# Performance work log

Hardware: AMD Instinct MI355X
Metric: run time of the kernel (lower is better)

The kernel has to match this reference:

```python
import jax, jax.numpy as jnp
import numpy as np

B, OBS, D_MODEL, D_STATE, D_CONV, EXPAND, ACT = 2048, 512, 1024, 16, 4, 2, 18
D_INNER = EXPAND * D_MODEL            # 2048
DT_RANK = (D_MODEL + 15) // 16        # 64

def setup_inputs() -> dict:
    key = jax.random.key(0)
    ks = jax.random.split(key, 20)
    s = 0.02
    return {
        "obs": jax.random.normal(ks[0], (B, OBS), jnp.float32),
        "conv_state": jax.random.normal(ks[1], (B, D_INNER, D_CONV), jnp.float32),
        "ssm_state": jax.random.normal(ks[2], (B, D_INNER, D_STATE), jnp.float32),
        # obs -> d_model projection
        "in_proj_w": jax.random.normal(ks[3], (D_MODEL, OBS), jnp.float32) * s,
        "in_proj_b": jnp.zeros((D_MODEL,), jnp.float32),
        # Mamba in_proj (no bias): d_model -> 2*d_inner (x and z)
        "mamba_in_w": jax.random.normal(ks[4], (2 * D_INNER, D_MODEL), jnp.float32) * s,
        # depthwise causal conv
        "conv_w": jax.random.normal(ks[5], (D_INNER, D_CONV), jnp.float32) * s,
        "conv_b": jnp.zeros((D_INNER,), jnp.float32),
        # x_proj (no bias): d_inner -> dt_rank + 2*d_state
        "x_proj_w": jax.random.normal(ks[6], (DT_RANK + 2 * D_STATE, D_INNER), jnp.float32) * s,
        # dt_proj: dt_rank -> d_inner
        "dt_w": jax.random.normal(ks[7], (D_INNER, DT_RANK), jnp.float32) * s,
        "dt_b": jax.random.normal(ks[8], (D_INNER,), jnp.float32) * s,
        # S4D-style A init: A_log = log(A), A in [1, d_state]
        "A_log": jnp.log(jnp.broadcast_to(jnp.arange(1, D_STATE + 1, dtype=jnp.float32), (D_INNER, D_STATE)) + 0.0),
        "D": jnp.ones((D_INNER,), jnp.float32),
        # out_proj (no bias): d_inner -> d_model
        "out_proj_w": jax.random.normal(ks[9], (D_MODEL, D_INNER), jnp.float32) * s,
        # actor / critic heads
        "pol_w": jax.random.normal(ks[10], (ACT, D_MODEL), jnp.float32) * s,
        "pol_b": jnp.zeros((ACT,), jnp.float32),
        "val_w": jax.random.normal(ks[11], (1, D_MODEL), jnp.float32) * s,
        "val_b": jnp.zeros((1,), jnp.float32),
    }

def _silu(x):
    return x * jax.nn.sigmoid(x)

def reference(obs, conv_state, ssm_state, in_proj_w, in_proj_b, mamba_in_w,
              conv_w, conv_b, x_proj_w, dt_w, dt_b, A_log, D, out_proj_w,
              pol_w, pol_b, val_w, val_b):
    # obs projection: [B, d_model]
    h = obs @ in_proj_w.T + in_proj_b
    # Mamba step (single timestep)
    xz = h @ mamba_in_w.T                        # [B, 2*d_inner]
    x, z = xz[:, :D_INNER], xz[:, D_INNER:]
    # causal depthwise conv via shifted conv_state buffer
    conv_state_new = jnp.concatenate([conv_state[:, :, 1:], x[:, :, None]], axis=-1)  # [B, d_inner, d_conv]
    x = _silu(jnp.sum(conv_state_new * conv_w[None], axis=-1) + conv_b)               # [B, d_inner]
    # input-dependent dt, B, C
    x_db = x @ x_proj_w.T                        # [B, dt_rank + 2*d_state]
    dt = x_db[:, :DT_RANK]
    Bmat = x_db[:, DT_RANK:DT_RANK + D_STATE]    # [B, d_state]
    Cmat = x_db[:, DT_RANK + D_STATE:]           # [B, d_state]
    dt = jax.nn.softplus(dt @ dt_w.T + dt_b)     # [B, d_inner]
    A = -jnp.exp(A_log)                          # [d_inner, d_state]
    dA = jnp.exp(dt[:, :, None] * A[None])       # [B, d_inner, d_state]
    dB = dt[:, :, None] * Bmat[:, None, :]       # [B, d_inner, d_state]
    ssm_state_new = ssm_state * dA + x[:, :, None] * dB
    y = jnp.einsum('bdn,bn->bd', ssm_state_new, Cmat) + D * x
    y = y * _silu(z)
    out = y @ out_proj_w.T                       # [B, d_model]
    logits = out @ pol_w.T + pol_b               # [B, action_dim]
    value = out @ val_w.T + val_b                # [B, 1]
    return logits, value, conv_state_new, ssm_state_new
```

## Files before the change

kernel.cpp:

```cpp
#include <hip/hip_runtime.h>
#include <hip/hip_bf16.h>
#include <math.h>


#define BATCH 2048
#define OBSD 512
#define DMODEL 1024
#define DINNER 2048
#define DSTATE 16
#define DTRANK 64
#define NACT 18

typedef __attribute__((ext_vector_type(8))) short shortx8;
typedef __attribute__((ext_vector_type(4))) float floatx4;

__device__ inline float sig_(float x) { return 1.f / (1.f + __expf(-x)); }

__device__ inline unsigned short bfc(float x) {
    __hip_bfloat16 h = __float2bfloat16(x);
    return *(unsigned short*)&h;
}

__device__ inline void store_bf4(unsigned short* dst, float4 v) {
    ushort4 u;
    u.x = bfc(v.x); u.y = bfc(v.y); u.z = bfc(v.z); u.w = bfc(v.w);
    *(ushort4*)dst = u;
}

__global__ __launch_bounds__(256) void convert_fold_kernel(
    const float* __restrict__ obs, const float* __restrict__ w1,
    const float* __restrict__ w2, const float* __restrict__ w3,
    const float* __restrict__ Alog, const float* __restrict__ opw,
    const float* __restrict__ pol_w, const float* __restrict__ val_w,
    unsigned short* __restrict__ obs_bf, unsigned short* __restrict__ w1_bf,
    unsigned short* __restrict__ w2_bf, unsigned short* __restrict__ w3_bf,
    float* __restrict__ A_neg, float* __restrict__ Wc)
{
    int blk = blockIdx.x;
    if (blk >= 5920) {
        __shared__ float hw[1024];
        int idx = blk - 5920;
        int j = idx % 19;
        int dblk = idx / 19;
        const float* src = (j < 18) ? (pol_w + j * 1024) : val_w;
        for (int t = threadIdx.x; t < 1024; t += 256) hw[t] = src[t];
        __syncthreads();
        int d = dblk * 256 + threadIdx.x;
        float acc = 0.f;
#pragma unroll 8
        for (int m = 0; m < 1024; ++m)
            acc += hw[m] * opw[(size_t)m * 2048 + d];
        Wc[j * 2048 + d] = acc;
        return;
    }
    int g = blk * 256 + threadIdx.x;
    if (g < 262144) {
        store_bf4(obs_bf + g * 4, ((const float4*)obs)[g]);
    } else if (g < 393216) {
        int t = g - 262144;
        store_bf4(w1_bf + t * 4, ((const float4*)w1)[t]);
    } else if (g < 1441792) {
        int t = g - 393216;
        store_bf4(w2_bf + t * 4, ((const float4*)w2)[t]);
    } else if (g < 1507328) {
        int t = g - 1441792;
        int e = t * 4;
        int n = e >> 11;
        int k = e & 2047;
        float4 v = {0.f, 0.f, 0.f, 0.f};
        if (n < 96) v = *(const float4*)(w3 + n * 2048 + k);
        store_bf4(w3_bf + e, v);
    } else {
        int t = g - 1507328;
        float4 v = ((const float4*)Alog)[t];
        float4 o = {-__expf(v.x), -__expf(v.y), -__expf(v.z), -__expf(v.w)};
        ((float4*)A_neg)[t] = o;
    }
}

__device__ __forceinline__ void stage_tile(
    const short* Abase, const short* Bbase, short* As, short* Bs,
    int K, int k0, int wave, int r0, int c0, int r1, int c1)
{
    __builtin_amdgcn_global_load_lds(
        (const __attribute__((address_space(1))) unsigned int*)(Abase + (size_t)r0 * K + k0 + c0),
        (__attribute__((address_space(3))) unsigned int*)(As + wave * 512), 16, 0, 0);
    __builtin_amdgcn_global_load_lds(
        (const __attribute__((address_space(1))) unsigned int*)(Abase + (size_t)r1 * K + k0 + c1),
        (__attribute__((address_space(3))) unsigned int*)(As + 2048 + wave * 512), 16, 0, 0);
    __builtin_amdgcn_global_load_lds(
        (const __attribute__((address_space(1))) unsigned int*)(Bbase + (size_t)r0 * K + k0 + c0),
        (__attribute__((address_space(3))) unsigned int*)(Bs + wave * 512), 16, 0, 0);
    __builtin_amdgcn_global_load_lds(
        (const __attribute__((address_space(1))) unsigned int*)(Bbase + (size_t)r1 * K + k0 + c1),
        (__attribute__((address_space(3))) unsigned int*)(Bs + 2048 + wave * 512), 16, 0, 0);
}

template <int BF16OUT, int BIAS, int SPLITK>
__global__ __launch_bounds__(256) void gemm_bt(
    const short* __restrict__ A, const short* __restrict__ Bm,
    void* __restrict__ Cout, const float* __restrict__ bias,
    int M, int N, int K, int ksplit_len)
{
    __shared__ short As[2][128 * 32];
    __shared__ short Bs[2][128 * 32];

    const int tid  = threadIdx.x;
    const int wave = tid >> 6;
    const int lane = tid & 63;
    const int quad = lane >> 4;
    const int l16  = lane & 15;
    const int wm   = (wave & 1) << 6;
    const int wn   = (wave >> 1) << 6;
    const int bm   = blockIdx.x;
    const int bn   = blockIdx.y;

    int kbeg = 0, kend = K;
    if (SPLITK) { kbeg = blockIdx.z * ksplit_len; kend = kbeg + ksplit_len; }

    floatx4 acc[4][4] = {};

    const int v0 = tid * 8;
    const int r0 = v0 >> 5, c0 = v0 & 31;
    const int v1 = (256 + tid) * 8;
    const int r1 = v1 >> 5, c1 = v1 & 31;

    const short* Abase = A + (size_t)bm * 128 * K;
    const short* Bbase = Bm + (size_t)bn * 128 * K;

    stage_tile(Abase, Bbase, As[0], Bs[0], K, kbeg, wave, r0, c0, r1, c1);
    __syncthreads();

    int cur = 0;
    for (int k0 = kbeg; k0 < kend; k0 += 32) {
        if (k0 + 32 < kend)
            stage_tile(Abase, Bbase, As[cur ^ 1], Bs[cur ^ 1], K, k0 + 32,
                       wave, r0, c0, r1, c1);
        shortx8 af[4], bfv[4];
#pragma unroll
        for (int i = 0; i < 4; ++i)
            af[i] = *(const shortx8*)(As[cur] + (wm + i * 16 + l16) * 32 + quad * 8);
#pragma unroll
        for (int j = 0; j < 4; ++j)
            bfv[j] = *(const shortx8*)(Bs[cur] + (wn + j * 16 + l16) * 32 + quad * 8);
#pragma unroll
        for (int i = 0; i < 4; ++i)
#pragma unroll
            for (int j = 0; j < 4; ++j)
                acc[i][j] = __builtin_amdgcn_mfma_f32_16x16x32_bf16(af[i], bfv[j], acc[i][j], 0, 0, 0);
        __syncthreads();
        cur ^= 1;
    }

    if (BF16OUT) {
        unsigned short* C = (unsigned short*)Cout;
#pragma unroll
        for (int i = 0; i < 4; ++i) {
            int gm = bm * 128 + wm + i * 16 + quad * 4;
#pragma unroll
            for (int j = 0; j < 4; ++j) {
                int gn = bn * 128 + wn + j * 16 + l16;
                float bv = BIAS ? bias[gn] : 0.f;
#pragma unroll
                for (int r = 0; r < 4; ++r)
                    C[(size_t)(gm + r) * N + gn] = bfc(acc[i][j][r] + bv);
            }
        }
    } else {
        float* C = (float*)Cout;
        if (SPLITK) C += (size_t)blockIdx.z * M * N;
#pragma unroll
        for (int i = 0; i < 4; ++i) {
            int gm = bm * 128 + wm + i * 16 + quad * 4;
#pragma unroll
            for (int j = 0; j < 4; ++j) {
                int gn = bn * 128 + wn + j * 16 + l16;
                float bv = BIAS ? bias[gn] : 0.f;
#pragma unroll
                for (int r = 0; r < 4; ++r)
                    C[(size_t)(gm + r) * N + gn] = acc[i][j][r] + bv;
            }
        }
    }
}

__global__ __launch_bounds__(256) void gemm_g2(
    const short* __restrict__ A, const short* __restrict__ Bm,
    const float* __restrict__ conv_state, const float* __restrict__ conv_w,
    const float* __restrict__ conv_b, float* __restrict__ conv_out,
    float* __restrict__ x_conv, unsigned short* __restrict__ x_conv_bf,
    float* __restrict__ zs, int K)
{
    __shared__ short As[2][128 * 32];
    __shared__ short Bs[2][128 * 32];

    const int tid  = threadIdx.x;
    const int wave = tid >> 6;
    const int lane = tid & 63;
    const int quad = lane >> 4;
    const int l16  = lane & 15;
    const int wm   = (wave & 1) << 6;
    const int wn   = (wave >> 1) << 6;
    const int bm   = blockIdx.x;
    const int bn   = blockIdx.y;

    floatx4 acc[4][4] = {};

    const int v0 = tid * 8;
    const int r0 = v0 >> 5, c0 = v0 & 31;
    const int v1 = (256 + tid) * 8;
    const int r1 = v1 >> 5, c1 = v1 & 31;

    const short* Abase = A + (size_t)bm * 128 * K;
    const short* Bbase = Bm + (size_t)bn * 128 * K;

    stage_tile(Abase, Bbase, As[0], Bs[0], K, 0, wave, r0, c0, r1, c1);
    __syncthreads();

    int cur = 0;
    for (int k0 = 0; k0 < K; k0 += 32) {
        if (k0 + 32 < K)
            stage_tile(Abase, Bbase, As[cur ^ 1], Bs[cur ^ 1], K, k0 + 32,
                       wave, r0, c0, r1, c1);
        shortx8 af[4], bfv[4];
#pragma unroll
        for (int i = 0; i < 4; ++i)
            af[i] = *(const shortx8*)(As[cur] + (wm + i * 16 + l16) * 32 + quad * 8);
#pragma unroll
        for (int j = 0; j < 4; ++j)
            bfv[j] = *(const shortx8*)(Bs[cur] + (wn + j * 16 + l16) * 32 + quad * 8);
#pragma unroll
        for (int i = 0; i < 4; ++i)
#pragma unroll
            for (int j = 0; j < 4; ++j)
                acc[i][j] = __builtin_amdgcn_mfma_f32_16x16x32_bf16(af[i], bfv[j], acc[i][j], 0, 0, 0);
        __syncthreads();
        cur ^= 1;
    }

    if (bn < 16) {
#pragma unroll
        for (int j = 0; j < 4; ++j) {
            int d = bn * 128 + wn + j * 16 + l16;
            float4 w4 = *(const float4*)(conv_w + d * 4);
            float cb = conv_b[d];
#pragma unroll
            for (int i = 0; i < 4; ++i) {
                int gm = bm * 128 + wm + i * 16 + quad * 4;
#pragma unroll
                for (int r = 0; r < 4; ++r) {
                    size_t idx = (size_t)(gm + r) * 2048 + d;
                    float xv = acc[i][j][r];
                    float4 cs = *(const float4*)(conv_state + idx * 4);
                    float s = cs.y * w4.x + cs.z * w4.y + cs.w * w4.z + xv * w4.w + cb;
                    float xc = s * sig_(s);
                    float4 outv = {cs.y, cs.z, cs.w, xv};
                    *(float4*)(conv_out + idx * 4) = outv;
                    x_conv[idx] = xc;
                    x_conv_bf[idx] = bfc(xc);
                }
            }
        }
    } else {
#pragma unroll
        for (int j = 0; j < 4; ++j) {
            int d = bn * 128 + wn + j * 16 + l16 - 2048;
#pragma unroll
            for (int i = 0; i < 4; ++i) {
                int gm = bm * 128 + wm + i * 16 + quad * 4;
#pragma unroll
                for (int r = 0; r < 4; ++r) {
                    float zv = acc[i][j][r];
                    zs[(size_t)(gm + r) * 2048 + d] = zv * sig_(zv);
                }
            }
        }
    }
}

__global__ __launch_bounds__(256) void dt_kernel(
    const float* __restrict__ part, const float* __restrict__ dt_w,
    const float* __restrict__ dt_b, float* __restrict__ dt_full,
    float* __restrict__ x_db)
{
    __shared__ float dtp[8][64];
    int tid = threadIdx.x;
    int b0 = blockIdx.y * 8;
    {
        int bb = tid >> 5, k = tid & 31;
        size_t base = ((size_t)(b0 + bb)) * 128;
        float s0 = 0.f, s1 = 0.f;
#pragma unroll
        for (int z = 0; z < 8; ++z) {
            s0 += part[(size_t)z * BATCH * 128 + base + k];
            s1 += part[(size_t)z * BATCH * 128 + base + k + 32];
        }
        dtp[bb][k]      = s0;
        dtp[bb][k + 32] = s1;
        if (blockIdx.x == 0) {
            float s2 = 0.f;
#pragma unroll
            for (int z = 0; z < 8; ++z)
                s2 += part[(size_t)z * BATCH * 128 + base + 64 + k];
            x_db[(b0 + bb) * 96 + 64 + k] = s2;
        }
    }
    __syncthreads();
    int d = blockIdx.x * 256 + tid;
    float acc[8];
    float bv = dt_b[d];
#pragma unroll
    for (int bb = 0; bb < 8; ++bb) acc[bb] = bv;
    const float4* w = (const float4*)(dt_w + d * 64);
#pragma unroll
    for (int k4 = 0; k4 < 16; ++k4) {
        float4 wv = w[k4];
#pragma unroll
        for (int bb = 0; bb < 8; ++bb) {
            acc[bb] += dtp[bb][k4 * 4 + 0] * wv.x + dtp[bb][k4 * 4 + 1] * wv.y +
                       dtp[bb][k4 * 4 + 2] * wv.z + dtp[bb][k4 * 4 + 3] * wv.w;
        }
    }
#pragma unroll
    for (int bb = 0; bb < 8; ++bb) {
        float a = acc[bb];
        float sp = a > 20.f ? a : log1pf(__expf(a));
        dt_full[(size_t)(b0 + bb) * 2048 + d] = sp;
    }
}

__global__ __launch_bounds__(256) void ssm_heads_kernel(
    const float* __restrict__ ssm_state, const float* __restrict__ x_conv,
    const float* __restrict__ dt_full, const float* __restrict__ zs,
    const float* __restrict__ x_db, const float* __restrict__ A_neg,
    const float* __restrict__ Dvec, const float* __restrict__ Wc,
    const float* __restrict__ pol_b, const float* __restrict__ val_b,
    float* __restrict__ ssm_out, float* __restrict__ logits,
    float* __restrict__ value)
{
    __shared__ float BC[32];
    __shared__ __align__(16) float yrow[2048];
    int b = blockIdx.x;
    int tid = threadIdx.x;
    if (tid < 32) BC[tid] = x_db[b * 96 + 64 + tid];
    __syncthreads();
    int q = tid & 3;
    int dl = tid >> 2;
    for (int r = 0; r < 32; ++r) {
        int d = r * 64 + dl;
        size_t idx = (size_t)b * 2048 + d;
        float x  = x_conv[idx];
        float dt = dt_full[idx];
        float xdt = x * dt;
        float4 s = *(const float4*)(ssm_state + idx * 16 + q * 4);
        float4 a = *(const float4*)(A_neg + (size_t)d * 16 + q * 4);
        float4 o;
        o.x = s.x * __expf(dt * a.x) + xdt * BC[q * 4 + 0];
        o.y = s.y * __expf(dt * a.y) + xdt * BC[q * 4 + 1];
        o.z = s.z * __expf(dt * a.z) + xdt * BC[q * 4 + 2];
        o.w = s.w * __expf(dt * a.w) + xdt * BC[q * 4 + 3];
        *(float4*)(ssm_out + idx * 16 + q * 4) = o;
        float p = o.x * BC[16 + q * 4 + 0] + o.y * BC[16 + q * 4 + 1] +
                  o.z * BC[16 + q * 4 + 2] + o.w * BC[16 + q * 4 + 3];
        p += __shfl_xor(p, 1);
        p += __shfl_xor(p, 2);
        if (q == 0) {
            float y = p + Dvec[d] * x;
            yrow[d] = y * zs[idx];
        }
    }
    __syncthreads();
    int wave = tid >> 6, lane = tid & 63;
    for (int j = wave; j < 19; j += 4) {
        const float4* w = (const float4*)(Wc + j * 2048);
        float p = 0.f;
        for (int k4 = lane; k4 < 512; k4 += 64) {
            float4 wv = w[k4];
            float4 rv = ((const float4*)yrow)[k4];
            p += rv.x * wv.x + rv.y * wv.y + rv.z * wv.z + rv.w * wv.w;
        }
#pragma unroll
        for (int off = 32; off; off >>= 1) p += __shfl_down(p, off);
        if (lane == 0) {
            if (j < 18) logits[b * NACT + j] = p + pol_b[j];
            else        value[b] = p + val_b[0];
        }
    }
}

extern "C" void kernel_launch(void* const* d_in, const int* in_sizes, int n_in,
                              void* d_out, int out_size, void* d_ws, size_t ws_size,
                              hipStream_t stream)
{
    const float* obs        = (const float*)d_in[0];
    const float* conv_state = (const float*)d_in[1];
    const float* ssm_state  = (const float*)d_in[2];
    const float* in_proj_w  = (const float*)d_in[3];
    const float* in_proj_b  = (const float*)d_in[4];
    const float* mamba_in_w = (const float*)d_in[5];
    const float* conv_w     = (const float*)d_in[6];
    const float* conv_b     = (const float*)d_in[7];
    const float* x_proj_w   = (const float*)d_in[8];
    const float* dt_w       = (const float*)d_in[9];
    const float* dt_b       = (const float*)d_in[10];
    const float* A_log      = (const float*)d_in[11];
    const float* Dvec       = (const float*)d_in[12];
    const float* out_proj_w = (const float*)d_in[13];
    const float* pol_w      = (const float*)d_in[14];
    const float* pol_b      = (const float*)d_in[15];
    const float* val_w      = (const float*)d_in[16];
    const float* val_b      = (const float*)d_in[17];

    char* ws = (char*)d_ws;
    unsigned short* obs_bf    = (unsigned short*)(ws + 0);
    unsigned short* w1_bf     = (unsigned short*)(ws + 2097152);
    unsigned short* w2_bf     = (unsigned short*)(ws + 3145728);
    unsigned short* w3_bf     = (unsigned short*)(ws + 11534336);
    float*          A_neg     = (float*)(ws + 12058624);
    unsigned short* h_bf      = (unsigned short*)(ws + 12189696);
    float*          x_conv    = (float*)(ws + 16384000);
    unsigned short* x_conv_bf = (unsigned short*)(ws + 33161216);
    float*          zs        = (float*)(ws + 41549824);
    float*          g3_part   = (float*)(ws + 58327040);
    float*          x_db      = (float*)(ws + 66715648);
    float*          dt_full   = (float*)(ws + 67502080);
    float*          Wc        = (float*)(ws + 84279296);
    if (ws_size < 84434944) return;

    float* logits   = (float*)d_out;
    float* value    = logits + (size_t)BATCH * NACT;
    float* conv_out = value + BATCH;
    float* ssm_out  = conv_out + (size_t)BATCH * DINNER * 4;

    convert_fold_kernel<<<6072, 256, 0, stream>>>(
        obs, in_proj_w, mamba_in_w, x_proj_w, A_log, out_proj_w, pol_w, val_w,
        obs_bf, w1_bf, w2_bf, w3_bf, A_neg, Wc);

    gemm_bt<1, 1, 0><<<dim3(16, 8), 256, 0, stream>>>(
        (const short*)obs_bf, (const short*)w1_bf, h_bf, in_proj_b, 2048, 1024, 512, 0);

    gemm_g2<<<dim3(16, 32), 256, 0, stream>>>(
        (const short*)h_bf, (const short*)w2_bf, conv_state, conv_w, conv_b,
        conv_out, x_conv, x_conv_bf, zs, 1024);

    gemm_bt<0, 0, 1><<<dim3(16, 1, 8), 256, 0, stream>>>(
        (const short*)x_conv_bf, (const short*)w3_bf, g3_part, nullptr, 2048, 128, 2048, 256);

    dt_kernel<<<dim3(8, 256), 256, 0, stream>>>(g3_part, dt_w, dt_b, dt_full, x_db);

    ssm_heads_kernel<<<2048, 256, 0, stream>>>(
        ssm_state, x_conv, dt_full, zs, x_db, A_neg, Dvec, Wc, pol_b, val_b,
        ssm_out, logits, value);
}
```

Before: 859.1 us.

## Split SSM update and heads into separate kernels with wider grid

Splits the fused SSM-plus-heads kernel into an SSM kernel launched over 16384 blocks and a separate heads kernel that reads y from a new workspace buffer. The split-K reduction of x_db moves into its own reduce kernel, so dt_kernel no longer redoes the partial sums in every block. The goal is more parallelism and memory-level concurrency in the bandwidth-bound SSM state update, which previously looped serially over 32 rows per batch block. In exchange it adds two kernel launches and a round trip of y (16 MB) through global memory.

```diff
diff --git a/kernel.cpp b/kernel.cpp
--- a/kernel.cpp
+++ b/kernel.cpp
@@ -278,32 +278,29 @@
     }
 }
 
+__global__ __launch_bounds__(256) void reduce_g3(
+    const float* __restrict__ part, float* __restrict__ x_db)
+{
+    int idx = blockIdx.x * 256 + threadIdx.x;
+    int b = idx / 96, n = idx - b * 96;
+    float s = 0.f;
+#pragma unroll
+    for (int z = 0; z < 8; ++z)
+        s += part[(size_t)z * BATCH * 128 + b * 128 + n];
+    x_db[idx] = s;
+}
+
 __global__ __launch_bounds__(256) void dt_kernel(
-    const float* __restrict__ part, const float* __restrict__ dt_w,
-    const float* __restrict__ dt_b, float* __restrict__ dt_full,
-    float* __restrict__ x_db)
+    const float* __restrict__ x_db, const float* __restrict__ dt_w,
+    const float* __restrict__ dt_b, float* __restrict__ dt_full)
 {
     __shared__ float dtp[8][64];
     int tid = threadIdx.x;
     int b0 = blockIdx.y * 8;
     {
         int bb = tid >> 5, k = tid & 31;
-        size_t base = ((size_t)(b0 + bb)) * 128;
-        float s0 = 0.f, s1 = 0.f;
-#pragma unroll
-        for (int z = 0; z < 8; ++z) {
-            s0 += part[(size_t)z * BATCH * 128 + base + k];
-            s1 += part[(size_t)z * BATCH * 128 + base + k + 32];
-        }
-        dtp[bb][k]      = s0;
-        dtp[bb][k + 32] = s1;
-        if (blockIdx.x == 0) {
-            float s2 = 0.f;
-#pragma unroll
-            for (int z = 0; z < 8; ++z)
-                s2 += part[(size_t)z * BATCH * 128 + base + 64 + k];
-            x_db[(b0 + bb) * 96 + 64 + k] = s2;
-        }
+        dtp[bb][k]      = x_db[(b0 + bb) * 96 + k];
+        dtp[bb][k + 32] = x_db[(b0 + bb) * 96 + k + 32];
     }
     __syncthreads();
     int d = blockIdx.x * 256 + tid;
@@ -329,46 +326,54 @@
     }
 }
 
-__global__ __launch_bounds__(256) void ssm_heads_kernel(
+__global__ __launch_bounds__(256) void ssm_kernel(
     const float* __restrict__ ssm_state, const float* __restrict__ x_conv,
     const float* __restrict__ dt_full, const float* __restrict__ zs,
     const float* __restrict__ x_db, const float* __restrict__ A_neg,
-    const float* __restrict__ Dvec, const float* __restrict__ Wc,
+    const float* __restrict__ Dvec, float* __restrict__ ssm_out,
+    float* __restrict__ y)
+{
+    const int q   = threadIdx.x & 3;
+    const int gid = blockIdx.x * 64 + (threadIdx.x >> 2);
+    const size_t QSTRIDE = (size_t)BATCH * DINNER / 4;
+#pragma unroll
+    for (int u = 0; u < 4; ++u) {
+        size_t idx = (size_t)gid + (size_t)u * QSTRIDE;
+        int b = (int)(idx >> 11);
+        int d = (int)(idx & 2047);
+        float xc  = x_conv[idx];
+        float dtv = dt_full[idx];
+        float zv  = zs[idx];
+        float Dd  = Dvec[d];
+        floatx4 Bv = *(const floatx4*)(x_db + b * 96 + 64 + q * 4);
+        floatx4 Cv = *(const floatx4*)(x_db + b * 96 + 80 + q * 4);
+        floatx4 s  = *(const floatx4*)(ssm_state + idx * 16 + q * 4);
+        floatx4 a  = *(const floatx4*)(A_neg + (size_t)d * 16 + q * 4);
+        float xdt = xc * dtv;
+        floatx4 o;
+        o.x = s.x * __expf(dtv * a.x) + xdt * Bv.x;
+        o.y = s.y * __expf(dtv * a.y) + xdt * Bv.y;
+        o.z = s.z * __expf(dtv * a.z) + xdt * Bv.z;
+        o.w = s.w * __expf(dtv * a.w) + xdt * Bv.w;
+        *(floatx4*)(ssm_out + idx * 16 + q * 4) = o;
+        float p = o.x * Cv.x + o.y * Cv.y + o.z * Cv.z + o.w * Cv.w;
+        p += __shfl_xor(p, 1);
+        p += __shfl_xor(p, 2);
+        if (q == 0) y[idx] = (p + Dd * xc) * zv;
+    }
+}
+
+__global__ __launch_bounds__(256) void heads_kernel(
+    const float* __restrict__ y, const float* __restrict__ Wc,
     const float* __restrict__ pol_b, const float* __restrict__ val_b,
-    float* __restrict__ ssm_out, float* __restrict__ logits,
-    float* __restrict__ value)
-{
-    __shared__ float BC[32];
-    __shared__ __align__(16) float yrow[2048];
+    float* __restrict__ logits, float* __restrict__ value)
+{
+    __shared__ __align__(16) float row[2048];
     int b = blockIdx.x;
     int tid = threadIdx.x;
-    if (tid < 32) BC[tid] = x_db[b * 96 + 64 + tid];
-    __syncthreads();
-    int q = tid & 3;
-    int dl = tid >> 2;
-    for (int r = 0; r < 32; ++r) {
-        int d = r * 64 + dl;
-        size_t idx = (size_t)b * 2048 + d;
-        float x  = x_conv[idx];
-        float dt = dt_full[idx];
-        float xdt = x * dt;
-        float4 s = *(const float4*)(ssm_state + idx * 16 + q * 4);
-        float4 a = *(const float4*)(A_neg + (size_t)d * 16 + q * 4);
-        float4 o;
-        o.x = s.x * __expf(dt * a.x) + xdt * BC[q * 4 + 0];
-        o.y = s.y * __expf(dt * a.y) + xdt * BC[q * 4 + 1];
-        o.z = s.z * __expf(dt * a.z) + xdt * BC[q * 4 + 2];
-        o.w = s.w * __expf(dt * a.w) + xdt * BC[q * 4 + 3];
-        *(float4*)(ssm_out + idx * 16 + q * 4) = o;
-        float p = o.x * BC[16 + q * 4 + 0] + o.y * BC[16 + q * 4 + 1] +
-                  o.z * BC[16 + q * 4 + 2] + o.w * BC[16 + q * 4 + 3];
-        p += __shfl_xor(p, 1);
-        p += __shfl_xor(p, 2);
-        if (q == 0) {
-            float y = p + Dvec[d] * x;
-            yrow[d] = y * zs[idx];
-        }
-    }
+    const float4* src = (const float4*)(y + (size_t)b * 2048);
+    ((float4*)row)[tid]       = src[tid];
+    ((float4*)row)[tid + 256] = src[tid + 256];
     __syncthreads();
     int wave = tid >> 6, lane = tid & 63;
     for (int j = wave; j < 19; j += 4) {
@@ -376,7 +381,7 @@
         float p = 0.f;
         for (int k4 = lane; k4 < 512; k4 += 64) {
             float4 wv = w[k4];
-            float4 rv = ((const float4*)yrow)[k4];
+            float4 rv = ((const float4*)row)[k4];
             p += rv.x * wv.x + rv.y * wv.y + rv.z * wv.z + rv.w * wv.w;
         }
 #pragma unroll
@@ -423,9 +428,10 @@
     float*          zs        = (float*)(ws + 41549824);
     float*          g3_part   = (float*)(ws + 58327040);
     float*          x_db      = (float*)(ws + 66715648);
-    float*          dt_full   = (float*)(ws + 67502080);
-    float*          Wc        = (float*)(ws + 84279296);
-    if (ws_size < 84434944) return;
+    float*          Wc        = (float*)(ws + 67502080);
+    float*          dt_full   = (float*)(ws + 67657728);
+    float*          yv        = (float*)(ws + 84434944);
+    if (ws_size < 101212160) return;
 
     float* logits   = (float*)d_out;
     float* value    = logits + (size_t)BATCH * NACT;
@@ -446,9 +452,12 @@
     gemm_bt<0, 0, 1><<<dim3(16, 1, 8), 256, 0, stream>>>(
         (const short*)x_conv_bf, (const short*)w3_bf, g3_part, nullptr, 2048, 128, 2048, 256);
 
-    dt_kernel<<<dim3(8, 256), 256, 0, stream>>>(g3_part, dt_w, dt_b, dt_full, x_db);
-
-    ssm_heads_kernel<<<2048, 256, 0, stream>>>(
-        ssm_state, x_conv, dt_full, zs, x_db, A_neg, Dvec, Wc, pol_b, val_b,
-        ssm_out, logits, value);
-}
+    reduce_g3<<<768, 256, 0, stream>>>(g3_part, x_db);
+
+    dt_kernel<<<dim3(8, 256), 256, 0, stream>>>(x_db, dt_w, dt_b, dt_full);
+
+    ssm_kernel<<<16384, 256, 0, stream>>>(
+        ssm_state, x_conv, dt_full, zs, x_db, A_neg, Dvec, ssm_out, yv);
+
+    heads_kernel<<<2048, 256, 0, stream>>>(yv, Wc, pol_b, val_b, logits, value);
+}
```

Result: faster. 826.9 us (-3.7%).
